# Kernel tuning notes

Measured on AMD Instinct MI355X. Metric: run time of the kernel, lower is better.

Reference implementation:

```python
import jax, jax.numpy as jnp
import numpy as np

N_NODES = 10000
N_EDGES = 50000
NUM_GENES = 1000
HEADS = 8
DIMS_IN = [256, 448 * 8, 384 * 8, 256 * 8]
DIMS_OUT = [448, 384, 256, NUM_GENES]
HEADS_L = [8, 8, 8, 1]


def _leaky_relu(x):
    return jnp.where(x >= 0, x, 0.2 * x)


def gat_conv(x, src, dst, n, W, a_src, a_dst, b, heads, c):
    # W: [heads*c, f_in]; a_src/a_dst: [heads, c]; b: [heads*c]
    h = (x @ W.T).reshape(n, heads, c)                      # [N,H,C]
    al_s = jnp.einsum('nhc,hc->nh', h, a_src)               # [N,H]
    al_d = jnp.einsum('nhc,hc->nh', h, a_dst)
    e = _leaky_relu(al_s[src] + al_d[dst])                  # [E,H]
    # segment softmax over incoming edges of each dst node
    m = jax.ops.segment_max(e, dst, num_segments=n)
    e = jnp.exp(e - m[dst])
    s = jax.ops.segment_sum(e, dst, num_segments=n)
    alpha = e / (s[dst] + 1e-16)
    out = jax.ops.segment_sum(h[src] * alpha[:, :, None], dst, num_segments=n)
    return out.reshape(n, heads * c) + b


def graph_ln(x, w, b):
    # PyG LayerNorm mode='graph': normalize over all node features of the graph
    mu = x.mean()
    var = ((x - mu) ** 2).mean()
    return (x - mu) * jax.lax.rsqrt(var + 1e-5) * w + b


def setup_inputs() -> dict:
    key = jax.random.key(0)
    ks = jax.random.split(key, 32)
    inp = {
        'x': jax.random.normal(ks[0], (N_NODES, DIMS_IN[0]), dtype=jnp.float32),
        'edge_index': jax.random.randint(ks[1], (2, N_EDGES), 0, N_NODES, dtype=jnp.int32),
    }
    ki = 2
    for li in range(4):
        h, c, fin = HEADS_L[li], DIMS_OUT[li], DIMS_IN[li]
        inp[f'W{li+1}'] = jax.random.normal(ks[ki], (h * c, fin), dtype=jnp.float32) * (fin ** -0.5); ki += 1
        inp[f'a_src{li+1}'] = jax.random.normal(ks[ki], (h, c), dtype=jnp.float32) * 0.1; ki += 1
        inp[f'a_dst{li+1}'] = jax.random.normal(ks[ki], (h, c), dtype=jnp.float32) * 0.1; ki += 1
        inp[f'b{li+1}'] = jnp.zeros((h * c,), dtype=jnp.float32)
        if li < 3:
            inp[f'ln{li+1}_w'] = jnp.ones((h * c,), dtype=jnp.float32)
            inp[f'ln{li+1}_b'] = jnp.zeros((h * c,), dtype=jnp.float32)
    return inp


def reference(x, edge_index,
              W1, a_src1, a_dst1, b1, ln1_w, ln1_b,
              W2, a_src2, a_dst2, b2, ln2_w, ln2_b,
              W3, a_src3, a_dst3, b3, ln3_w, ln3_b,
              W4, a_src4, a_dst4, b4):
    n = x.shape[0]
    loops = jnp.arange(n, dtype=edge_index.dtype)
    src = jnp.concatenate([edge_index[0], loops])  # add_self_loops=True (PyG default)
    dst = jnp.concatenate([edge_index[1], loops])
    h = jax.nn.relu(gat_conv(x, src, dst, n, W1, a_src1, a_dst1, b1, 8, 448))
    h = graph_ln(h, ln1_w, ln1_b)
    h = jax.nn.relu(gat_conv(h, src, dst, n, W2, a_src2, a_dst2, b2, 8, 384))
    h = graph_ln(h, ln2_w, ln2_b)
    h = jax.nn.relu(gat_conv(h, src, dst, n, W3, a_src3, a_dst3, b3, 8, 256))
    h = graph_ln(h, ln3_w, ln3_b)
    out = gat_conv(h, src, dst, n, W4, a_src4, a_dst4, b4, 1, NUM_GENES)
    return out
```

## Files before the change

### kernel.cpp

```cpp
#include <hip/hip_runtime.h>
#include <hip/hip_bf16.h>

typedef _Float16 h8 __attribute__((ext_vector_type(8)));
typedef _Float16 h4 __attribute__((ext_vector_type(4)));
typedef __attribute__((ext_vector_type(4))) float facc4;

__device__ __forceinline__ unsigned fenc(float v) {
  unsigned b = __float_as_uint(v);
  return (b & 0x80000000u) ? ~b : (b | 0x80000000u);
}
__device__ __forceinline__ float fdec(unsigned u) {
  return (u & 0x80000000u) ? __uint_as_float(u & 0x7fffffffu) : __uint_as_float(~u);
}
__device__ __forceinline__ void gload16(const void* g, void* l) {
  __builtin_amdgcn_global_load_lds((const __attribute__((address_space(1))) void*)g,
                                   (__attribute__((address_space(3))) void*)l, 16, 0, 0);
}

__global__ void f2h_k(const float* __restrict__ in, unsigned short* __restrict__ out, int n4) {
  int i = blockIdx.x * 256 + threadIdx.x;
  int stride = gridDim.x * 256;
  for (; i < n4; i += stride) {
    float4 v = ((const float4*)in)[i];
    h4 o;
    o[0] = (_Float16)v.x; o[1] = (_Float16)v.y; o[2] = (_Float16)v.z; o[3] = (_Float16)v.w;
    ((h4*)out)[i] = o;
  }
}

__global__ __launch_bounds__(256) void gemm_f16(
    const unsigned short* __restrict__ A, const unsigned short* __restrict__ B,
    unsigned short* __restrict__ Hout,
    float* __restrict__ als, float* __restrict__ ald,
    const float* __restrict__ a_src, const float* __restrict__ a_dst,
    int M, int Nn, int K, int C, int H, int gx, int nwg) {
  __shared__ unsigned short As[128 * 32];
  __shared__ unsigned short Bs[128 * 32];
  const int tid = threadIdx.x, lane = tid & 63, wv = tid >> 6;

  int lin = blockIdx.x;
  int q = nwg >> 3, r = nwg & 7;
  int xcd = lin & 7, idx = lin >> 3;
  int swz = (xcd < r) ? (xcd * (q + 1) + idx) : (r * (q + 1) + (xcd - r) * q + idx);
  const int bx = swz % gx, by = swz / gx;
  const int brow = by * 128, bcol = bx * 128;
  const int wr = wv >> 1, wc = wv & 1;

  const int sr = (2 * wv) * 16 + (lane >> 2);
  const int kk = (lane & 3) * 8;
  int ar0 = brow + sr;      if (ar0 > M - 1)  ar0 = M - 1;
  int ar1 = brow + sr + 16; if (ar1 > M - 1)  ar1 = M - 1;
  int bc0 = bcol + sr;      if (bc0 > Nn - 1) bc0 = Nn - 1;
  int bc1 = bcol + sr + 16; if (bc1 > Nn - 1) bc1 = Nn - 1;
  const unsigned short* pa0 = A + (size_t)ar0 * K + kk;
  const unsigned short* pa1 = A + (size_t)ar1 * K + kk;
  const unsigned short* pb0 = B + (size_t)bc0 * K + kk;
  const unsigned short* pb1 = B + (size_t)bc1 * K + kk;
  unsigned short* asd0 = &As[(2 * wv) * 512];
  unsigned short* asd1 = &As[(2 * wv + 1) * 512];
  unsigned short* bsd0 = &Bs[(2 * wv) * 512];
  unsigned short* bsd1 = &Bs[(2 * wv + 1) * 512];

  facc4 acc[4][4] = {};
  const int r0 = wr * 64 + (lane & 15);
  const int c0 = wc * 64 + (lane & 15);
  const int ko = (lane >> 4) * 8;

  const int nK = K >> 5;
  for (int kt = 0; kt < nK; ++kt) {
    gload16(pa0, asd0); gload16(pa1, asd1);
    gload16(pb0, bsd0); gload16(pb1, bsd1);
    pa0 += 32; pa1 += 32; pb0 += 32; pb1 += 32;
    __syncthreads();
    h8 af[4], bf[4];
#pragma unroll
    for (int i = 0; i < 4; ++i) af[i] = *(const h8*)&As[(r0 + i * 16) * 32 + ko];
#pragma unroll
    for (int j = 0; j < 4; ++j) bf[j] = *(const h8*)&Bs[(c0 + j * 16) * 32 + ko];
#pragma unroll
    for (int i = 0; i < 4; ++i)
#pragma unroll
      for (int j = 0; j < 4; ++j)
        acc[i][j] = __builtin_amdgcn_mfma_f32_16x16x32_f16(af[i], bf[j], acc[i][j], 0, 0, 0);
    __syncthreads();
  }

  const int rbase = brow + wr * 64 + ((lane >> 4) << 2);
  const int cbase = bcol + wc * 64 + (lane & 15);

  float asv[4], adv[4];
#pragma unroll
  for (int j = 0; j < 4; ++j) {
    int col = cbase + j * 16;
    bool ok = col < Nn;
    asv[j] = ok ? a_src[col] : 0.f;
    adv[j] = ok ? a_dst[col] : 0.f;
  }
  const int hh = (bcol + wc * 64) / C;
#pragma unroll
  for (int i = 0; i < 4; ++i)
#pragma unroll
    for (int r2 = 0; r2 < 4; ++r2) {
      float s1 = 0.f, s2 = 0.f;
#pragma unroll
      for (int j = 0; j < 4; ++j) { float v = acc[i][j][r2]; s1 += v * asv[j]; s2 += v * adv[j]; }
#pragma unroll
      for (int m = 1; m < 16; m <<= 1) { s1 += __shfl_xor(s1, m); s2 += __shfl_xor(s2, m); }
      int row = rbase + i * 16 + r2;
      if ((lane & 15) == 0 && row < M) {
        atomicAdd(&als[row * H + hh], s1);
        atomicAdd(&ald[row * H + hh], s2);
      }
    }

#pragma unroll
  for (int i = 0; i < 4; ++i)
#pragma unroll
    for (int j = 0; j < 4; ++j) {
      int col = cbase + j * 16;
      if (col >= Nn) continue;
#pragma unroll
      for (int r2 = 0; r2 < 4; ++r2) {
        int row = rbase + i * 16 + r2;
        if (row < M) {
          _Float16 hv = (_Float16)acc[i][j][r2];
          Hout[(size_t)row * Nn + col] = *(unsigned short*)&hv;
        }
      }
    }
}

__global__ void count_deg_k(const int* __restrict__ ei, int* __restrict__ deg, int Ereal, int Etot) {
  int e = blockIdx.x * 256 + threadIdx.x;
  if (e >= Etot) return;
  int dst = (e < Ereal) ? ei[Ereal + e] : (e - Ereal);
  atomicAdd(&deg[dst], 1);
}

__global__ void scan_k(const int* __restrict__ deg, int* __restrict__ rowptr, int n) {
  __shared__ int sums[1024];
  int t = threadIdx.x;
  int base = t * 10;
  int loc[10]; int s = 0;
#pragma unroll
  for (int i = 0; i < 10; ++i) { int idx = base + i; int d = (idx < n) ? deg[idx] : 0; loc[i] = s; s += d; }
  sums[t] = s;
  __syncthreads();
  for (int off = 1; off < 1024; off <<= 1) {
    int add = (t >= off) ? sums[t - off] : 0;
    __syncthreads();
    sums[t] += add;
    __syncthreads();
  }
  int excl = sums[t] - s;
#pragma unroll
  for (int i = 0; i < 10; ++i) { int idx = base + i; if (idx < n) rowptr[idx] = excl + loc[i]; }
  if (t == 1023) rowptr[n] = sums[1023];
}

__global__ void scatter_k(const int* __restrict__ ei, const int* __restrict__ rowptr,
                          int* __restrict__ fill, int* __restrict__ esrc, int* __restrict__ eid,
                          int Ereal, int Etot) {
  int e = blockIdx.x * 256 + threadIdx.x;
  if (e >= Etot) return;
  int src = (e < Ereal) ? ei[e] : (e - Ereal);
  int dst = (e < Ereal) ? ei[Ereal + e] : (e - Ereal);
  int pos = rowptr[dst] + atomicAdd(&fill[dst], 1);
  esrc[pos] = src; eid[pos] = e;
}

template <int H>
__global__ void attn_max_k(const int* __restrict__ ei, const float* __restrict__ als,
                           const float* __restrict__ ald, unsigned* __restrict__ mu,
                           int Ereal, int Etot) {
  int idx = blockIdx.x * 256 + threadIdx.x;
  if (idx >= Etot * H) return;
  int e = idx / H, h = idx % H;
  int src = (e < Ereal) ? ei[e] : (e - Ereal);
  int dst = (e < Ereal) ? ei[Ereal + e] : (e - Ereal);
  float v = als[src * H + h] + ald[dst * H + h];
  v = (v >= 0.f) ? v : 0.2f * v;
  atomicMax(&mu[dst * H + h], fenc(v));
}

template <int H>
__global__ void attn_expsum_k(const int* __restrict__ ei, const float* __restrict__ als,
                              const float* __restrict__ ald, const unsigned* __restrict__ mu,
                              float* __restrict__ ealpha, float* __restrict__ ss,
                              int Ereal, int Etot) {
  int idx = blockIdx.x * 256 + threadIdx.x;
  if (idx >= Etot * H) return;
  int e = idx / H, h = idx % H;
  int src = (e < Ereal) ? ei[e] : (e - Ereal);
  int dst = (e < Ereal) ? ei[Ereal + e] : (e - Ereal);
  float v = als[src * H + h] + ald[dst * H + h];
  v = (v >= 0.f) ? v : 0.2f * v;
  float p = expf(v - fdec(mu[dst * H + h]));
  ealpha[idx] = p;
  atomicAdd(&ss[dst * H + h], p);
}

template <int H, bool FP32OUT, bool STATS>
__global__ __launch_bounds__(256) void aggregate_k(
    const unsigned short* __restrict__ hfp, const float* __restrict__ ealpha,
    const float* __restrict__ ss, const int* __restrict__ rowptr,
    const int* __restrict__ esrc, const int* __restrict__ eid,
    const float* __restrict__ bias, void* __restrict__ outv,
    float* __restrict__ lnsums, int C, int F) {
  const int node = blockIdx.x;
  const int tid = threadIdx.x;
  int beg = rowptr[node];
  int deg = rowptr[node + 1] - beg;
  if (deg > 128) deg = 128;
  __shared__ int   s_src[128];
  __shared__ float s_al[128 * H];
  for (int d = tid; d < deg; d += 256) {
    s_src[d] = esrc[beg + d];
    int e = eid[beg + d];
#pragma unroll
    for (int h = 0; h < H; ++h)
      s_al[d * H + h] = ealpha[e * H + h] / (ss[node * H + h] + 1e-16f);
  }
  __syncthreads();
  float s1 = 0.f, s2 = 0.f;
  const int F8 = F >> 3;
  for (int c8 = tid; c8 < F8; c8 += 256) {
    int f0 = c8 * 8;
    int h = f0 / C;
    float a[8];
    float4 b0 = *(const float4*)(bias + f0);
    float4 b1 = *(const float4*)(bias + f0 + 4);
    a[0] = b0.x; a[1] = b0.y; a[2] = b0.z; a[3] = b0.w;
    a[4] = b1.x; a[5] = b1.y; a[6] = b1.z; a[7] = b1.w;
    for (int d = 0; d < deg; ++d) {
      float al = s_al[d * H + h];
      h8 hv = *(const h8*)(hfp + (size_t)s_src[d] * F + f0);
#pragma unroll
      for (int j = 0; j < 8; ++j) a[j] = fmaf(al, (float)hv[j], a[j]);
    }
    size_t i = (size_t)node * F + f0;
    if (FP32OUT) {
      float4 o0 = {a[0], a[1], a[2], a[3]};
      float4 o1 = {a[4], a[5], a[6], a[7]};
      *(float4*)((float*)outv + i) = o0;
      *(float4*)((float*)outv + i + 4) = o1;
    } else {
      h8 o;
#pragma unroll
      for (int j = 0; j < 8; ++j) o[j] = (_Float16)a[j];
      *(h8*)((unsigned short*)outv + i) = o;
    }
    if (STATS) {
#pragma unroll
      for (int j = 0; j < 8; ++j) { float v = a[j] > 0.f ? a[j] : 0.f; s1 += v; s2 += v * v; }
    }
  }
  if (STATS) {
#pragma unroll
    for (int m = 32; m; m >>= 1) { s1 += __shfl_down(s1, m); s2 += __shfl_down(s2, m); }
    __shared__ float r1[4], r2[4];
    if ((tid & 63) == 0) { r1[tid >> 6] = s1; r2[tid >> 6] = s2; }
    __syncthreads();
    if (tid == 0) {
      atomicAdd(&lnsums[0], r1[0] + r1[1] + r1[2] + r1[3]);
      atomicAdd(&lnsums[1], r2[0] + r2[1] + r2[2] + r2[3]);
    }
  }
}

__global__ void ln_apply_k(unsigned short* __restrict__ x, const float* __restrict__ sums,
                           const float* __restrict__ w, const float* __restrict__ b,
                           int total8, int F8, float inv_count) {
  int i8 = blockIdx.x * 256 + threadIdx.x;
  if (i8 >= total8) return;
  float mu = sums[0] * inv_count;
  float var = sums[1] * inv_count - mu * mu;
  float istd = rsqrtf(var + 1e-5f);
  int f0 = (i8 % F8) * 8;
  h8 hv = *(h8*)(x + (size_t)i8 * 8);
  float4 w0 = *(const float4*)(w + f0), w1 = *(const float4*)(w + f0 + 4);
  float4 b0 = *(const float4*)(b + f0), b1 = *(const float4*)(b + f0 + 4);
  float wv[8] = {w0.x, w0.y, w0.z, w0.w, w1.x, w1.y, w1.z, w1.w};
  float bv[8] = {b0.x, b0.y, b0.z, b0.w, b1.x, b1.y, b1.z, b1.w};
  h8 o;
#pragma unroll
  for (int j = 0; j < 8; ++j) {
    float v = (float)hv[j]; v = v > 0.f ? v : 0.f;
    o[j] = (_Float16)((v - mu) * istd * wv[j] + bv[j]);
  }
  *(h8*)(x + (size_t)i8 * 8) = o;
}

extern "C" void kernel_launch(void* const* d_in, const int* in_sizes, int n_in,
                              void* d_out, int out_size, void* d_ws, size_t ws_size,
                              hipStream_t stream) {
  const int N = 10000, Ereal = 50000, Etot = 60000;
  const float* x  = (const float*)d_in[0];
  const int*   ei = (const int*)d_in[1];
  const float* W[4]    = {(const float*)d_in[2],  (const float*)d_in[8],  (const float*)d_in[14], (const float*)d_in[20]};
  const float* asrc[4] = {(const float*)d_in[3],  (const float*)d_in[9],  (const float*)d_in[15], (const float*)d_in[21]};
  const float* adst[4] = {(const float*)d_in[4],  (const float*)d_in[10], (const float*)d_in[16], (const float*)d_in[22]};
  const float* bias[4] = {(const float*)d_in[5],  (const float*)d_in[11], (const float*)d_in[17], (const float*)d_in[23]};
  const float* lnw[3]  = {(const float*)d_in[6],  (const float*)d_in[12], (const float*)d_in[18]};
  const float* lnb[3]  = {(const float*)d_in[7],  (const float*)d_in[13], (const float*)d_in[19]};

  const int fin[4]  = {256, 3584, 3072, 2048};
  const int fout[4] = {3584, 3072, 2048, 1000};
  const int CH[4]   = {448, 384, 256, 1000};

  size_t off = 0;
  char* base = (char*)d_ws;
  auto alloc = [&](size_t bytes) -> void* {
    void* p = base + off;
    off += (bytes + 255) & ~(size_t)255;
    return p;
  };
  unsigned short* xh  = (unsigned short*)alloc((size_t)N * 3584 * 2);
  unsigned short* hh  = (unsigned short*)alloc((size_t)N * 3584 * 2);
  unsigned short* wh  = (unsigned short*)alloc((size_t)3072 * 3584 * 2);
  float*          als    = (float*)alloc((size_t)N * 8 * 4);
  float*          ald    = (float*)alloc((size_t)N * 8 * 4);
  unsigned*       mu_    = (unsigned*)alloc((size_t)N * 8 * 4);
  float*          ssum   = (float*)alloc((size_t)N * 8 * 4);
  float*          ealpha = (float*)alloc((size_t)Etot * 8 * 4);
  int*            deg    = (int*)alloc((size_t)N * 4);
  int*            fill   = (int*)alloc((size_t)N * 4);
  int*            rowptr = (int*)alloc((size_t)(N + 1) * 4);
  int*            esrc   = (int*)alloc((size_t)Etot * 4);
  int*            eid    = (int*)alloc((size_t)Etot * 4);
  float*          lnsums = (float*)alloc(256);

  auto cdiv = [](int a, int b) { return (a + b - 1) / b; };

  hipMemsetAsync(deg, 0, (size_t)N * 4, stream);
  hipMemsetAsync(fill, 0, (size_t)N * 4, stream);
  count_deg_k<<<cdiv(Etot, 256), 256, 0, stream>>>(ei, deg, Ereal, Etot);
  scan_k<<<1, 1024, 0, stream>>>(deg, rowptr, N);
  scatter_k<<<cdiv(Etot, 256), 256, 0, stream>>>(ei, rowptr, fill, esrc, eid, Ereal, Etot);

  {
    int n4 = (N * fin[0]) / 4;
    f2h_k<<<min(2048, cdiv(n4, 256)), 256, 0, stream>>>(x, xh, n4);
  }

  for (int l = 0; l < 4; ++l) {
    const int K = fin[l], Fo = fout[l], C = CH[l];
    const int H = (l == 3) ? 1 : 8;

    {
      int n4 = (Fo * K) / 4;
      f2h_k<<<min(2048, cdiv(n4, 256)), 256, 0, stream>>>(W[l], wh, n4);
    }

    hipMemsetAsync(als, 0, (size_t)N * H * 4, stream);
    hipMemsetAsync(ald, 0, (size_t)N * H * 4, stream);

    {
      int gx = cdiv(Fo, 128), gy = cdiv(N, 128);
      int nwg = gx * gy;
      gemm_f16<<<nwg, 256, 0, stream>>>(xh, wh, hh, als, ald, asrc[l], adst[l],
                                        N, Fo, K, C, H, gx, nwg);
    }

    hipMemsetAsync(mu_, 0, (size_t)N * H * 4, stream);
    hipMemsetAsync(ssum, 0, (size_t)N * H * 4, stream);
    if (H == 8) {
      attn_max_k<8><<<cdiv(Etot * 8, 256), 256, 0, stream>>>(ei, als, ald, mu_, Ereal, Etot);
      attn_expsum_k<8><<<cdiv(Etot * 8, 256), 256, 0, stream>>>(ei, als, ald, mu_, ealpha, ssum, Ereal, Etot);
    } else {
      attn_max_k<1><<<cdiv(Etot, 256), 256, 0, stream>>>(ei, als, ald, mu_, Ereal, Etot);
      attn_expsum_k<1><<<cdiv(Etot, 256), 256, 0, stream>>>(ei, als, ald, mu_, ealpha, ssum, Ereal, Etot);
    }

    if (l < 3) {
      hipMemsetAsync(lnsums, 0, 8, stream);
      aggregate_k<8, false, true><<<N, 256, 0, stream>>>(hh, ealpha, ssum, rowptr, esrc, eid,
                                                         bias[l], xh, lnsums, C, Fo);
      int F8 = Fo >> 3;
      int total8 = N * F8;
      ln_apply_k<<<cdiv(total8, 256), 256, 0, stream>>>(xh, lnsums, lnw[l], lnb[l],
                                                        total8, F8, 1.0f / (float)(N * Fo));
    } else {
      aggregate_k<1, true, false><<<N, 256, 0, stream>>>(hh, ealpha, ssum, rowptr, esrc, eid,
                                                         bias[l], d_out, nullptr, C, Fo);
    }
  }
}
```

Baseline: 1.707 ms.

## Triple-buffer swizzled GEMM tiles and fuse segment softmax into aggregation

The GEMM moves to 512 threads with 256x128 tiles, 64-wide K steps, an XOR-swizzled LDS layout and a three-stage global_load_lds pipeline using explicit vmcnt waits and MFMA priority hints. This hides load latency and cuts LDS bank conflicts. Separately, the atomic max and exp-sum kernels are removed. Each aggregation block now computes the leaky-relu scores, per-head max, exp and normalisation for its destination node in shared memory, which drops the edge-id array, several atomics and extra launches. The per-node softmax runs serially on H threads and the GEMM's LDS footprint grows, which may limit occupancy.

```diff
diff --git a/kernel.cpp b/kernel.cpp
--- a/kernel.cpp
+++ b/kernel.cpp
@@ -1,17 +1,9 @@
 #include <hip/hip_runtime.h>
-#include <hip/hip_bf16.h>
 
 typedef _Float16 h8 __attribute__((ext_vector_type(8)));
 typedef _Float16 h4 __attribute__((ext_vector_type(4)));
 typedef __attribute__((ext_vector_type(4))) float facc4;
 
-__device__ __forceinline__ unsigned fenc(float v) {
-  unsigned b = __float_as_uint(v);
-  return (b & 0x80000000u) ? ~b : (b | 0x80000000u);
-}
-__device__ __forceinline__ float fdec(unsigned u) {
-  return (u & 0x80000000u) ? __uint_as_float(u & 0x7fffffffu) : __uint_as_float(~u);
-}
 __device__ __forceinline__ void gload16(const void* g, void* l) {
   __builtin_amdgcn_global_load_lds((const __attribute__((address_space(1))) void*)g,
                                    (__attribute__((address_space(3))) void*)l, 16, 0, 0);
@@ -28,14 +20,13 @@
   }
 }
 
-__global__ __launch_bounds__(256) void gemm_f16(
+__global__ __launch_bounds__(512, 2) void gemm_f16(
     const unsigned short* __restrict__ A, const unsigned short* __restrict__ B,
     unsigned short* __restrict__ Hout,
     float* __restrict__ als, float* __restrict__ ald,
     const float* __restrict__ a_src, const float* __restrict__ a_dst,
     int M, int Nn, int K, int C, int H, int gx, int nwg) {
-  __shared__ unsigned short As[128 * 32];
-  __shared__ unsigned short Bs[128 * 32];
+  __shared__ unsigned short lds[3 * 24576];
   const int tid = threadIdx.x, lane = tid & 63, wv = tid >> 6;
 
   int lin = blockIdx.x;
@@ -43,46 +34,76 @@
   int xcd = lin & 7, idx = lin >> 3;
   int swz = (xcd < r) ? (xcd * (q + 1) + idx) : (r * (q + 1) + (xcd - r) * q + idx);
   const int bx = swz % gx, by = swz / gx;
-  const int brow = by * 128, bcol = bx * 128;
+  const int brow = by * 256, bcol = bx * 128;
   const int wr = wv >> 1, wc = wv & 1;
 
-  const int sr = (2 * wv) * 16 + (lane >> 2);
-  const int kk = (lane & 3) * 8;
-  int ar0 = brow + sr;      if (ar0 > M - 1)  ar0 = M - 1;
-  int ar1 = brow + sr + 16; if (ar1 > M - 1)  ar1 = M - 1;
-  int bc0 = bcol + sr;      if (bc0 > Nn - 1) bc0 = Nn - 1;
-  int bc1 = bcol + sr + 16; if (bc1 > Nn - 1) bc1 = Nn - 1;
-  const unsigned short* pa0 = A + (size_t)ar0 * K + kk;
-  const unsigned short* pa1 = A + (size_t)ar1 * K + kk;
-  const unsigned short* pb0 = B + (size_t)bc0 * K + kk;
-  const unsigned short* pb1 = B + (size_t)bc1 * K + kk;
-  unsigned short* asd0 = &As[(2 * wv) * 512];
-  unsigned short* asd1 = &As[(2 * wv + 1) * 512];
-  unsigned short* bsd0 = &Bs[(2 * wv) * 512];
-  unsigned short* bsd1 = &Bs[(2 * wv + 1) * 512];
+  const int lr = lane >> 3;
+  const int gslot = (lane & 7) ^ lr;
+  const unsigned short* pa[4]; int ldsA[4];
+#pragma unroll
+  for (int i = 0; i < 4; ++i) {
+    int rl = wv * 32 + i * 8 + lr;
+    int rg = brow + rl; if (rg > M - 1) rg = M - 1;
+    pa[i] = A + (size_t)rg * K + gslot * 8;
+    ldsA[i] = (wv * 32 + i * 8) * 64;
+  }
+  const unsigned short* pb[2]; int ldsB[2];
+#pragma unroll
+  for (int i = 0; i < 2; ++i) {
+    int rl = wv * 16 + i * 8 + lr;
+    int rg = bcol + rl; if (rg > Nn - 1) rg = Nn - 1;
+    pb[i] = B + (size_t)rg * K + gslot * 8;
+    ldsB[i] = 16384 + (wv * 16 + i * 8) * 64;
+  }
+
+  const int ra0 = wr * 64 + (lane & 15);
+  const int rb0 = wc * 64 + (lane & 15);
+  const int g16 = lane >> 4;
+  const int lx = lane & 7;
 
   facc4 acc[4][4] = {};
-  const int r0 = wr * 64 + (lane & 15);
-  const int c0 = wc * 64 + (lane & 15);
-  const int ko = (lane >> 4) * 8;
-
-  const int nK = K >> 5;
-  for (int kt = 0; kt < nK; ++kt) {
-    gload16(pa0, asd0); gload16(pa1, asd1);
-    gload16(pb0, bsd0); gload16(pb1, bsd1);
-    pa0 += 32; pa1 += 32; pb0 += 32; pb1 += 32;
-    __syncthreads();
-    h8 af[4], bf[4];
-#pragma unroll
-    for (int i = 0; i < 4; ++i) af[i] = *(const h8*)&As[(r0 + i * 16) * 32 + ko];
-#pragma unroll
-    for (int j = 0; j < 4; ++j) bf[j] = *(const h8*)&Bs[(c0 + j * 16) * 32 + ko];
-#pragma unroll
-    for (int i = 0; i < 4; ++i)
-#pragma unroll
-      for (int j = 0; j < 4; ++j)
-        acc[i][j] = __builtin_amdgcn_mfma_f32_16x16x32_f16(af[i], bf[j], acc[i][j], 0, 0, 0);
-    __syncthreads();
+  const int nt = K >> 6;
+
+  auto STAGE = [&](int kt, int buf) {
+    const int bo = buf * 24576;
+#pragma unroll
+    for (int i = 0; i < 4; ++i) gload16(pa[i] + kt * 64, &lds[bo + ldsA[i]]);
+#pragma unroll
+    for (int i = 0; i < 2; ++i) gload16(pb[i] + kt * 64, &lds[bo + ldsB[i]]);
+  };
+
+  STAGE(0, 0);
+  STAGE(1, 1);
+  asm volatile("s_waitcnt vmcnt(6)" ::: "memory");
+  __builtin_amdgcn_s_barrier();
+  asm volatile("" ::: "memory");
+
+  int cb = 0, sb = 2;
+  for (int kt = 0; kt < nt; ++kt) {
+    if (kt + 2 < nt) STAGE(kt + 2, sb);
+    const int bo = cb * 24576;
+#pragma unroll
+    for (int kk = 0; kk < 2; ++kk) {
+      const int slot = (kk * 4 + g16) ^ lx;
+      h8 af[4], bf[4];
+#pragma unroll
+      for (int i = 0; i < 4; ++i) af[i] = *(const h8*)&lds[bo + (ra0 + i * 16) * 64 + slot * 8];
+#pragma unroll
+      for (int j = 0; j < 4; ++j) bf[j] = *(const h8*)&lds[bo + 16384 + (rb0 + j * 16) * 64 + slot * 8];
+      __builtin_amdgcn_s_setprio(1);
+#pragma unroll
+      for (int i = 0; i < 4; ++i)
+#pragma unroll
+        for (int j = 0; j < 4; ++j)
+          acc[i][j] = __builtin_amdgcn_mfma_f32_16x16x32_f16(af[i], bf[j], acc[i][j], 0, 0, 0);
+      __builtin_amdgcn_s_setprio(0);
+    }
+    if (kt + 2 < nt) asm volatile("s_waitcnt vmcnt(6)" ::: "memory");
+    else             asm volatile("s_waitcnt vmcnt(0)" ::: "memory");
+    __builtin_amdgcn_s_barrier();
+    asm volatile("" ::: "memory");
+    cb = (cb == 2) ? 0 : cb + 1;
+    sb = (sb == 2) ? 0 : sb + 1;
   }
 
   const int rbase = brow + wr * 64 + ((lane >> 4) << 2);
@@ -159,52 +180,21 @@
 }
 
 __global__ void scatter_k(const int* __restrict__ ei, const int* __restrict__ rowptr,
-                          int* __restrict__ fill, int* __restrict__ esrc, int* __restrict__ eid,
+                          int* __restrict__ fill, int* __restrict__ esrc,
                           int Ereal, int Etot) {
   int e = blockIdx.x * 256 + threadIdx.x;
   if (e >= Etot) return;
   int src = (e < Ereal) ? ei[e] : (e - Ereal);
   int dst = (e < Ereal) ? ei[Ereal + e] : (e - Ereal);
   int pos = rowptr[dst] + atomicAdd(&fill[dst], 1);
-  esrc[pos] = src; eid[pos] = e;
-}
-
-template <int H>
-__global__ void attn_max_k(const int* __restrict__ ei, const float* __restrict__ als,
-                           const float* __restrict__ ald, unsigned* __restrict__ mu,
-                           int Ereal, int Etot) {
-  int idx = blockIdx.x * 256 + threadIdx.x;
-  if (idx >= Etot * H) return;
-  int e = idx / H, h = idx % H;
-  int src = (e < Ereal) ? ei[e] : (e - Ereal);
-  int dst = (e < Ereal) ? ei[Ereal + e] : (e - Ereal);
-  float v = als[src * H + h] + ald[dst * H + h];
-  v = (v >= 0.f) ? v : 0.2f * v;
-  atomicMax(&mu[dst * H + h], fenc(v));
-}
-
-template <int H>
-__global__ void attn_expsum_k(const int* __restrict__ ei, const float* __restrict__ als,
-                              const float* __restrict__ ald, const unsigned* __restrict__ mu,
-                              float* __restrict__ ealpha, float* __restrict__ ss,
-                              int Ereal, int Etot) {
-  int idx = blockIdx.x * 256 + threadIdx.x;
-  if (idx >= Etot * H) return;
-  int e = idx / H, h = idx % H;
-  int src = (e < Ereal) ? ei[e] : (e - Ereal);
-  int dst = (e < Ereal) ? ei[Ereal + e] : (e - Ereal);
-  float v = als[src * H + h] + ald[dst * H + h];
-  v = (v >= 0.f) ? v : 0.2f * v;
-  float p = expf(v - fdec(mu[dst * H + h]));
-  ealpha[idx] = p;
-  atomicAdd(&ss[dst * H + h], p);
+  esrc[pos] = src;
 }
 
 template <int H, bool FP32OUT, bool STATS>
 __global__ __launch_bounds__(256) void aggregate_k(
-    const unsigned short* __restrict__ hfp, const float* __restrict__ ealpha,
-    const float* __restrict__ ss, const int* __restrict__ rowptr,
-    const int* __restrict__ esrc, const int* __restrict__ eid,
+    const unsigned short* __restrict__ hfp,
+    const float* __restrict__ als, const float* __restrict__ ald,
+    const int* __restrict__ rowptr, const int* __restrict__ esrc,
     const float* __restrict__ bias, void* __restrict__ outv,
     float* __restrict__ lnsums, int C, int F) {
   const int node = blockIdx.x;
@@ -213,15 +203,30 @@
   int deg = rowptr[node + 1] - beg;
   if (deg > 128) deg = 128;
   __shared__ int   s_src[128];
-  __shared__ float s_al[128 * H];
+  __shared__ float s_p[128][H];
+  __shared__ float s_inv[H];
+  float aldv[H];
+#pragma unroll
+  for (int h = 0; h < H; ++h) aldv[h] = ald[node * H + h];
   for (int d = tid; d < deg; d += 256) {
-    s_src[d] = esrc[beg + d];
-    int e = eid[beg + d];
-#pragma unroll
-    for (int h = 0; h < H; ++h)
-      s_al[d * H + h] = ealpha[e * H + h] / (ss[node * H + h] + 1e-16f);
+    int s = esrc[beg + d];
+    s_src[d] = s;
+#pragma unroll
+    for (int h = 0; h < H; ++h) {
+      float v = als[s * H + h] + aldv[h];
+      s_p[d][h] = (v >= 0.f) ? v : 0.2f * v;
+    }
   }
   __syncthreads();
+  if (tid < H) {
+    float m = -1e30f;
+    for (int d = 0; d < deg; ++d) m = fmaxf(m, s_p[d][tid]);
+    float s = 0.f;
+    for (int d = 0; d < deg; ++d) { float p = __expf(s_p[d][tid] - m); s_p[d][tid] = p; s += p; }
+    s_inv[tid] = 1.f / (s + 1e-16f);
+  }
+  __syncthreads();
+
   float s1 = 0.f, s2 = 0.f;
   const int F8 = F >> 3;
   for (int c8 = tid; c8 < F8; c8 += 256) {
@@ -233,7 +238,7 @@
     a[0] = b0.x; a[1] = b0.y; a[2] = b0.z; a[3] = b0.w;
     a[4] = b1.x; a[5] = b1.y; a[6] = b1.z; a[7] = b1.w;
     for (int d = 0; d < deg; ++d) {
-      float al = s_al[d * H + h];
+      float al = s_p[d][h] * s_inv[h];
       h8 hv = *(const h8*)(hfp + (size_t)s_src[d] * F + f0);
 #pragma unroll
       for (int j = 0; j < 8; ++j) a[j] = fmaf(al, (float)hv[j], a[j]);
@@ -320,14 +325,10 @@
   unsigned short* wh  = (unsigned short*)alloc((size_t)3072 * 3584 * 2);
   float*          als    = (float*)alloc((size_t)N * 8 * 4);
   float*          ald    = (float*)alloc((size_t)N * 8 * 4);
-  unsigned*       mu_    = (unsigned*)alloc((size_t)N * 8 * 4);
-  float*          ssum   = (float*)alloc((size_t)N * 8 * 4);
-  float*          ealpha = (float*)alloc((size_t)Etot * 8 * 4);
   int*            deg    = (int*)alloc((size_t)N * 4);
   int*            fill   = (int*)alloc((size_t)N * 4);
   int*            rowptr = (int*)alloc((size_t)(N + 1) * 4);
   int*            esrc   = (int*)alloc((size_t)Etot * 4);
-  int*            eid    = (int*)alloc((size_t)Etot * 4);
   float*          lnsums = (float*)alloc(256);
 
   auto cdiv = [](int a, int b) { return (a + b - 1) / b; };
@@ -336,7 +337,7 @@
   hipMemsetAsync(fill, 0, (size_t)N * 4, stream);
   count_deg_k<<<cdiv(Etot, 256), 256, 0, stream>>>(ei, deg, Ereal, Etot);
   scan_k<<<1, 1024, 0, stream>>>(deg, rowptr, N);
-  scatter_k<<<cdiv(Etot, 256), 256, 0, stream>>>(ei, rowptr, fill, esrc, eid, Ereal, Etot);
+  scatter_k<<<cdiv(Etot, 256), 256, 0, stream>>>(ei, rowptr, fill, esrc, Ereal, Etot);
 
   {
     int n4 = (N * fin[0]) / 4;
@@ -352,36 +353,25 @@
       f2h_k<<<min(2048, cdiv(n4, 256)), 256, 0, stream>>>(W[l], wh, n4);
     }
 
-    hipMemsetAsync(als, 0, (size_t)N * H * 4, stream);
-    hipMemsetAsync(ald, 0, (size_t)N * H * 4, stream);
+    hipMemsetAsync(als, 0, (size_t)N * 8 * 4 * 2, stream);
 
     {
-      int gx = cdiv(Fo, 128), gy = cdiv(N, 128);
+      int gx = cdiv(Fo, 128), gy = cdiv(N, 256);
       int nwg = gx * gy;
-      gemm_f16<<<nwg, 256, 0, stream>>>(xh, wh, hh, als, ald, asrc[l], adst[l],
+      gemm_f16<<<nwg, 512, 0, stream>>>(xh, wh, hh, als, ald, asrc[l], adst[l],
                                         N, Fo, K, C, H, gx, nwg);
-    }
-
-    hipMemsetAsync(mu_, 0, (size_t)N * H * 4, stream);
-    hipMemsetAsync(ssum, 0, (size_t)N * H * 4, stream);
-    if (H == 8) {
-      attn_max_k<8><<<cdiv(Etot * 8, 256), 256, 0, stream>>>(ei, als, ald, mu_, Ereal, Etot);
-      attn_expsum_k<8><<<cdiv(Etot * 8, 256), 256, 0, stream>>>(ei, als, ald, mu_, ealpha, ssum, Ereal, Etot);
-    } else {
-      attn_max_k<1><<<cdiv(Etot, 256), 256, 0, stream>>>(ei, als, ald, mu_, Ereal, Etot);
-      attn_expsum_k<1><<<cdiv(Etot, 256), 256, 0, stream>>>(ei, als, ald, mu_, ealpha, ssum, Ereal, Etot);
     }
 
     if (l < 3) {
       hipMemsetAsync(lnsums, 0, 8, stream);
-      aggregate_k<8, false, true><<<N, 256, 0, stream>>>(hh, ealpha, ssum, rowptr, esrc, eid,
+      aggregate_k<8, false, true><<<N, 256, 0, stream>>>(hh, als, ald, rowptr, esrc,
                                                          bias[l], xh, lnsums, C, Fo);
       int F8 = Fo >> 3;
       int total8 = N * F8;
       ln_apply_k<<<cdiv(total8, 256), 256, 0, stream>>>(xh, lnsums, lnw[l], lnb[l],
                                                         total8, F8, 1.0f / (float)(N * Fo));
     } else {
-      aggregate_k<1, true, false><<<N, 256, 0, stream>>>(hh, ealpha, ssum, rowptr, esrc, eid,
+      aggregate_k<1, true, false><<<N, 256, 0, stream>>>(hh, als, ald, rowptr, esrc,
                                                          bias[l], d_out, nullptr, C, Fo);
     }
   }
```

Result: faster. 1.577 ms (-7.6%).
